# Optimization experiments

Measured on AMD Instinct MI355X. Metric: run time of the kernel, lower is better.

Reference implementation:

```python
import jax, jax.numpy as jnp
import numpy as np

N = 4000      # number_of_sensors
D_IN = 128    # input feature dim
D_OUT = 128   # output feature dim
E_DIM = 16    # node embedding dim
B = 8         # batch size


def setup_inputs() -> dict:
    key = jax.random.key(0)
    k_x, k_e1, k_e2, k_w = jax.random.split(key, 4)
    x = jax.random.normal(k_x, (B, N, D_IN), dtype=jnp.float32)
    E1 = jax.random.normal(k_e1, (N, E_DIM), dtype=jnp.float32)
    E2 = jax.random.normal(k_e2, (N, E_DIM), dtype=jnp.float32)
    W = jax.random.normal(k_w, (D_IN, D_OUT), dtype=jnp.float32) * (1.0 / np.sqrt(D_IN))
    b = jnp.zeros((D_OUT,), dtype=jnp.float32)
    return {"x": x, "E1": E1, "E2": E2, "W": W, "b": b}


def reference(x, E1, E2, W, b):
    # Adaptive adjacency from node embeddings: A = softmax(relu(E1 @ E2^T), axis=-1)
    logits = jax.nn.relu(jnp.einsum('nd,md->nm', E1, E2))  # [N, N]
    adj = jax.nn.softmax(logits, axis=-1)                  # row-normalized adjacency
    # Graph aggregation then feature transform: relu(A @ X @ W + b)
    agg = jnp.einsum('nm,bmf->bnf', adj, x)                # [B, N, D_IN]
    out = jax.nn.relu(jnp.einsum('bnf,fo->bno', agg, W) + b)  # [B, N, D_OUT]
    return out
```

## Files before the change

kernel.cpp:

```cpp
#include <hip/hip_runtime.h>
#include <hip/hip_bf16.h>

#define NSEN 4000
#define NP   4096
#define DIN  128
#define DOUT 128
#define EDIM 16
#define BATCH 8

typedef __attribute__((ext_vector_type(8))) short bf16x8;
typedef __attribute__((ext_vector_type(4))) float f32x4;

__device__ __forceinline__ unsigned short f2bf(float f) {
  unsigned int u = __float_as_uint(f);
  unsigned int r = (u + 0x7FFFu + ((u >> 16) & 1u)) >> 16;
  return (unsigned short)r;
}
__device__ __forceinline__ float bf2f(unsigned short s) {
  unsigned int u = ((unsigned int)s) << 16;
  return __uint_as_float(u);
}

__device__ __forceinline__ void gl_lds16(const void* g, void* l) {
  __builtin_amdgcn_global_load_lds((const __attribute__((address_space(1))) void*)g,
                                   (__attribute__((address_space(3))) void*)l, 16, 0, 0);
}

__global__ __launch_bounds__(512) void k_prep(const float* __restrict__ E1,
                                              const float* __restrict__ E2,
                                              const float* __restrict__ W,
                                              const float* __restrict__ x,
                                              unsigned short* __restrict__ adjp,
                                              float* __restrict__ rinv,
                                              unsigned short* __restrict__ yt) {
  __shared__ float rsum[8][16];
  __shared__ __align__(16) unsigned short pool[34816];
  const int bx = blockIdx.x;
  const int tid = threadIdx.x;
  const int lane = tid & 63, wv = tid >> 6;
  const int lr = lane & 15, lq = lane >> 4;

  if (bx >= 250) {
    unsigned short* wlds = pool;
    unsigned short* ylds = pool + 17408;
    {
      const int fr = tid >> 5;
      const int o4 = tid & 31;
#pragma unroll
      for (int r8 = 0; r8 < 8; r8++) {
        const int f = fr + r8 * 16;
        float4 w4 = *(const float4*)&W[(size_t)f * DOUT + o4 * 4];
        wlds[(o4 * 4 + 0) * 136 + f] = f2bf(w4.x);
        wlds[(o4 * 4 + 1) * 136 + f] = f2bf(w4.y);
        wlds[(o4 * 4 + 2) * 136 + f] = f2bf(w4.z);
        wlds[(o4 * 4 + 3) * 136 + f] = f2bf(w4.w);
      }
    }
    __syncthreads();

    const int yi = bx - 250;
    const int b  = yi >> 5;
    const int m0 = (yi & 31) * 128;
    const int mh = wv >> 2;
    const int os = wv & 3;

    bf16x8 af[2][4];
#pragma unroll
    for (int ot = 0; ot < 2; ot++) {
      const int ob = os * 32 + ot * 16 + lr;
#pragma unroll
      for (int ks = 0; ks < 4; ks++)
        af[ot][ks] = *(const bf16x8*)&wlds[ob * 136 + ks * 32 + lq * 8];
    }

#pragma unroll
    for (int mt = 0; mt < 4; mt++) {
      const int mloc = mh * 64 + mt * 16;
      const int m = m0 + mloc + lr;
      bf16x8 bx8[4];
      if (m < NSEN) {
        const float* xp = &x[((size_t)b * NSEN + m) * DIN + lq * 8];
#pragma unroll
        for (int ks = 0; ks < 4; ks++) {
          float4 v0 = *(const float4*)(xp + ks * 32);
          float4 v1 = *(const float4*)(xp + ks * 32 + 4);
          bx8[ks][0] = (short)f2bf(v0.x); bx8[ks][1] = (short)f2bf(v0.y);
          bx8[ks][2] = (short)f2bf(v0.z); bx8[ks][3] = (short)f2bf(v0.w);
          bx8[ks][4] = (short)f2bf(v1.x); bx8[ks][5] = (short)f2bf(v1.y);
          bx8[ks][6] = (short)f2bf(v1.z); bx8[ks][7] = (short)f2bf(v1.w);
        }
      } else {
#pragma unroll
        for (int ks = 0; ks < 4; ks++)
#pragma unroll
          for (int j = 0; j < 8; j++) bx8[ks][j] = 0;
      }
#pragma unroll
      for (int ot = 0; ot < 2; ot++) {
        f32x4 c = (f32x4){0.f, 0.f, 0.f, 0.f};
#pragma unroll
        for (int ks = 0; ks < 4; ks++)
          c = __builtin_amdgcn_mfma_f32_16x16x32_bf16(af[ot][ks], bx8[ks], c, 0, 0, 0);
#pragma unroll
        for (int i = 0; i < 4; i++)
          ylds[(os * 32 + ot * 16 + lq * 4 + i) * 136 + mloc + lr] = f2bf(c[i]);
      }
    }
    __syncthreads();
#pragma unroll
    for (int s2 = 0; s2 < 4; s2++) {
      int c = s2 * 512 + tid;
      int row = c >> 4;
      int mc = c & 15;
      *(bf16x8*)&yt[(size_t)(b * 128 + row) * NP + m0 + mc * 8] =
          *(const bf16x8*)&ylds[row * 136 + mc * 8];
    }
    return;
  }

  const int n0 = bx * 16;

  float a[8];
  {
    const float* e1p = &E1[(size_t)(n0 + lr) * EDIM + (lq & 1) * 8];
    *(float4*)&a[0] = *(const float4*)e1p;
    *(float4*)&a[4] = *(const float4*)(e1p + 4);
  }
  bf16x8 af1, af2;
#pragma unroll
  for (int j = 0; j < 8; j++) {
    unsigned short hs = f2bf(a[j]);
    af1[j] = (short)hs;
    float lo = a[j] - bf2f(hs);
    af2[j] = (lq < 2) ? (short)f2bf(lo) : (short)0;
  }

  float rs[4] = {0.f, 0.f, 0.f, 0.f};
  for (int t = wv; t < NSEN / 16; t += 8) {
    const int m = t * 16 + lr;
    float bv[8];
    const float* e2p = &E2[(size_t)m * EDIM + (lq & 1) * 8];
    *(float4*)&bv[0] = *(const float4*)e2p;
    *(float4*)&bv[4] = *(const float4*)(e2p + 4);
    bf16x8 bfrag;
#pragma unroll
    for (int j = 0; j < 8; j++) {
      unsigned short hs = f2bf(bv[j]);
      if (lq < 2) bfrag[j] = (short)hs;
      else        bfrag[j] = (short)f2bf(bv[j] - bf2f(hs));
    }
    f32x4 c = (f32x4){0.f, 0.f, 0.f, 0.f};
    c = __builtin_amdgcn_mfma_f32_16x16x32_bf16(af1, bfrag, c, 0, 0, 0);
    c = __builtin_amdgcn_mfma_f32_16x16x32_bf16(af2, bfrag, c, 0, 0, 0);
#pragma unroll
    for (int i = 0; i < 4; i++) {
      float p = __expf(fmaxf(c[i], 0.f));
      rs[i] += p;
      adjp[(size_t)(n0 + lq * 4 + i) * NP + t * 16 + lr] = f2bf(p);
    }
  }
  for (int i = tid; i < 16 * (NP - NSEN); i += 512) {
    int r = i / (NP - NSEN), c = i % (NP - NSEN);
    adjp[(size_t)(n0 + r) * NP + NSEN + c] = 0;
  }
#pragma unroll
  for (int i = 0; i < 4; i++) {
    rs[i] += __shfl_xor(rs[i], 1, 64);
    rs[i] += __shfl_xor(rs[i], 2, 64);
    rs[i] += __shfl_xor(rs[i], 4, 64);
    rs[i] += __shfl_xor(rs[i], 8, 64);
  }
  if (lr == 0) {
#pragma unroll
    for (int i = 0; i < 4; i++) rsum[wv][lq * 4 + i] = rs[i];
  }
  __syncthreads();
  if (tid < 16) {
    float s = 0.f;
#pragma unroll
    for (int w = 0; w < 8; w++) s += rsum[w][tid];
    rinv[n0 + tid] = 1.0f / s;
  }
}

__global__ __launch_bounds__(512, 2) void k_gemm(const unsigned short* __restrict__ A,
                                                 const unsigned short* __restrict__ Bt,
                                                 unsigned short* __restrict__ part,
                                                 int nsteps) {
  __shared__ __align__(16) unsigned short smem[65536];
  unsigned short* tA0 = smem;
  unsigned short* tB0 = smem + 32768;
  const int tid = threadIdx.x;
  const int lane = tid & 63, wv = tid >> 6;
  const int wr = wv >> 2, wcn = wv & 3;
  const int lr = lane & 15, lq = lane >> 4;
  const int kh = blockIdx.x >> 4;
  const int m0 = (blockIdx.x & 15) * 256;
  const int n0c = blockIdx.y * 256;
  const int kb0 = kh * nsteps * 64;

  f32x4 acc[8][4];
#pragma unroll
  for (int p = 0; p < 8; p++)
#pragma unroll
    for (int q = 0; q < 4; q++) acc[p][q] = (f32x4){0.f, 0.f, 0.f, 0.f};

#define STAGE2(bufi, kb, s)                                                             \
  {                                                                                     \
    int idx = (s) * 512 + tid;                                                          \
    int row = idx >> 3;                                                                 \
    int kc = ((idx & 7) ^ (row & 7)) << 3;                                              \
    gl_lds16(&A[(size_t)(m0 + row) * NP + (kb) + kc], &tA0[(bufi)*16384 + idx*8]);      \
    gl_lds16(&Bt[(size_t)(n0c + row) * NP + (kb) + kc], &tB0[(bufi)*16384 + idx*8]);    \
  }

  STAGE2(0, kb0, 0); STAGE2(0, kb0, 1); STAGE2(0, kb0, 2); STAGE2(0, kb0, 3);

  for (int it = 0; it < nsteps; ++it) {
    const int cur = it & 1;
    const int nxt = cur ^ 1;
    const int kbn = kb0 + (it + 1) * 64;
    const bool pf = (it < nsteps - 1);
    bf16x8 bf[4];

#pragma unroll
    for (int ks = 0; ks < 2; ks++) {
      if (ks == 0) {
        if (pf) STAGE2(nxt, kbn, 0);
        if (it == 0) { asm volatile("s_waitcnt vmcnt(0)" ::: "memory"); }
        else if (pf) { asm volatile("s_waitcnt vmcnt(2)" ::: "memory"); }
        else         { asm volatile("s_waitcnt vmcnt(0)" ::: "memory"); }
        __builtin_amdgcn_s_barrier();
      } else {
        if (pf) STAGE2(nxt, kbn, 2);
      }
      {
        const int koff = (ks * 32 + lq * 8) ^ ((lr & 7) << 3);
        bf16x8 af[4];
#pragma unroll
        for (int p = 0; p < 4; p++)
          af[p] = *(const bf16x8*)&tA0[cur * 16384 + (wr * 128 + p * 16 + lr) * 64 + koff];
#pragma unroll
        for (int q = 0; q < 4; q++)
          bf[q] = *(const bf16x8*)&tB0[cur * 16384 + (wcn * 64 + q * 16 + lr) * 64 + koff];
        if (ks == 1) __builtin_amdgcn_s_barrier();
        asm volatile("s_waitcnt lgkmcnt(0)" ::: "memory");
        __builtin_amdgcn_sched_barrier(0);
        __builtin_amdgcn_s_setprio(1);
#pragma unroll
        for (int p = 0; p < 4; p++)
#pragma unroll
          for (int q = 0; q < 4; q++)
            acc[p][q] = __builtin_amdgcn_mfma_f32_16x16x32_bf16(af[p], bf[q], acc[p][q], 0, 0, 0);
        __builtin_amdgcn_s_setprio(0);
        __builtin_amdgcn_s_barrier();
      }
      {
        if (pf) STAGE2(nxt, kbn, (ks == 0) ? 1 : 3);
        const int koff = (ks * 32 + lq * 8) ^ ((lr & 7) << 3);
        bf16x8 af[4];
#pragma unroll
        for (int p = 0; p < 4; p++)
          af[p] = *(const bf16x8*)&tA0[cur * 16384 + (wr * 128 + (4 + p) * 16 + lr) * 64 + koff];
        __builtin_amdgcn_s_barrier();
        asm volatile("s_waitcnt lgkmcnt(0)" ::: "memory");
        __builtin_amdgcn_sched_barrier(0);
        __builtin_amdgcn_s_setprio(1);
#pragma unroll
        for (int p = 0; p < 4; p++)
#pragma unroll
          for (int q = 0; q < 4; q++)
            acc[4 + p][q] = __builtin_amdgcn_mfma_f32_16x16x32_bf16(af[p], bf[q], acc[4 + p][q], 0, 0, 0);
        __builtin_amdgcn_s_setprio(0);
        __builtin_amdgcn_s_barrier();
      }
    }
  }
#undef STAGE2

  unsigned short* pdst = part + ((size_t)kh << 22);
#pragma unroll
  for (int p = 0; p < 8; p++)
#pragma unroll
    for (int q = 0; q < 4; q++) {
      const int col = n0c + wcn * 64 + q * 16 + lr;
#pragma unroll
      for (int i = 0; i < 4; i++) {
        const int row = m0 + wr * 128 + p * 16 + lq * 4 + i;
        pdst[(size_t)row * 1024 + col] = f2bf(acc[p][q][i]);
      }
    }
}

__global__ __launch_bounds__(256) void k_fin(const unsigned short* __restrict__ part,
                                             const float* __restrict__ rinv,
                                             const float* __restrict__ bias,
                                             float* __restrict__ out, int ksl) {
  const int tid = threadIdx.x;
  const int nl = tid >> 4;
  const int ch = tid & 15;
  const int n  = blockIdx.x * 16 + nl;
  const int b  = blockIdx.y;
  const int j  = b * 128 + ch * 8;

  float s[8] = {0.f, 0.f, 0.f, 0.f, 0.f, 0.f, 0.f, 0.f};
  for (int kh = 0; kh < ksl; kh++) {
    bf16x8 pv = *(const bf16x8*)&part[((size_t)kh << 22) + (size_t)n * 1024 + j];
#pragma unroll
    for (int jj = 0; jj < 8; jj++) s[jj] += bf2f((unsigned short)pv[jj]);
  }
  const float rv = rinv[n];
  float4 bb0 = *(const float4*)&bias[ch * 8];
  float4 bb1 = *(const float4*)&bias[ch * 8 + 4];
  float r[8];
#pragma unroll
  for (int jj = 0; jj < 8; jj++) {
    float bbj = (jj < 4) ? ((const float*)&bb0)[jj] : ((const float*)&bb1)[jj - 4];
    r[jj] = fmaxf(s[jj] * rv + bbj, 0.f);
  }
  float* op = &out[((size_t)b * NSEN + n) * DOUT + ch * 8];
  *(float4*)op       = make_float4(r[0], r[1], r[2], r[3]);
  *(float4*)(op + 4) = make_float4(r[4], r[5], r[6], r[7]);
}

extern "C" void kernel_launch(void* const* d_in, const int* in_sizes, int n_in,
                              void* d_out, int out_size, void* d_ws, size_t ws_size,
                              hipStream_t stream) {
  const float* x    = (const float*)d_in[0];
  const float* E1   = (const float*)d_in[1];
  const float* E2   = (const float*)d_in[2];
  const float* W    = (const float*)d_in[3];
  const float* bias = (const float*)d_in[4];
  float* out = (float*)d_out;

  char* ws = (char*)d_ws;
  unsigned short* adjp = (unsigned short*)(ws);
  unsigned short* yt   = (unsigned short*)(ws + 33554432);
  float*          rinv = (float*)(ws + 33554432 + 8388608);
  unsigned short* part = (unsigned short*)(ws + 33554432 + 8388608 + 16384);

  const size_t need4 = 33554432ull + 8388608 + 16384 + 4ull * 8388608;
  const int KS = (ws_size >= need4) ? 4 : 2;
  const int nsteps = 64 / KS;

  k_prep<<<dim3(506), dim3(512), 0, stream>>>(E1, E2, W, x, adjp, rinv, yt);
  k_gemm<<<dim3(KS * 16, 4), dim3(512), 0, stream>>>(adjp, yt, part, nsteps);
  k_fin<<<dim3(250, BATCH), dim3(256), 0, stream>>>(part, rinv, bias, out, KS);
}
```

Measured before the change: 79.28 us.

## Switch GEMM mainloop to triple-buffered K=32 stages with one barrier per step

Replaces the double-buffered K=64 LDS pipeline in the adjacency GEMM with a three-slot ring of K=32 tiles. Loads run two steps ahead, with a new XOR swizzle for 32-wide rows. Each iteration now has a single barrier instead of several. The split-K factor is also forced to 4 without checking the workspace size, which risks overrunning the buffer if the workspace is small.

```diff
diff --git a/kernel.cpp b/kernel.cpp
--- a/kernel.cpp
+++ b/kernel.cpp
@@ -187,9 +187,9 @@
                                                  const unsigned short* __restrict__ Bt,
                                                  unsigned short* __restrict__ part,
                                                  int nsteps) {
-  __shared__ __align__(16) unsigned short smem[65536];
+  __shared__ __align__(16) unsigned short smem[49152];
   unsigned short* tA0 = smem;
-  unsigned short* tB0 = smem + 32768;
+  unsigned short* tB0 = smem + 24576;
   const int tid = threadIdx.x;
   const int lane = tid & 63, wv = tid >> 6;
   const int wr = wv >> 2, wcn = wv & 3;
@@ -197,7 +197,7 @@
   const int kh = blockIdx.x >> 4;
   const int m0 = (blockIdx.x & 15) * 256;
   const int n0c = blockIdx.y * 256;
-  const int kb0 = kh * nsteps * 64;
+  const int kb0 = kh * nsteps * 32;
 
   f32x4 acc[8][4];
 #pragma unroll
@@ -205,78 +205,81 @@
 #pragma unroll
     for (int q = 0; q < 4; q++) acc[p][q] = (f32x4){0.f, 0.f, 0.f, 0.f};
 
-#define STAGE2(bufi, kb, s)                                                             \
+#define STAGE_A(sl, kb, s)                                                              \
   {                                                                                     \
     int idx = (s) * 512 + tid;                                                          \
-    int row = idx >> 3;                                                                 \
-    int kc = ((idx & 7) ^ (row & 7)) << 3;                                              \
-    gl_lds16(&A[(size_t)(m0 + row) * NP + (kb) + kc], &tA0[(bufi)*16384 + idx*8]);      \
-    gl_lds16(&Bt[(size_t)(n0c + row) * NP + (kb) + kc], &tB0[(bufi)*16384 + idx*8]);    \
-  }
-
-  STAGE2(0, kb0, 0); STAGE2(0, kb0, 1); STAGE2(0, kb0, 2); STAGE2(0, kb0, 3);
-
+    int row = idx >> 2;                                                                 \
+    int kc = (((idx & 3) ^ ((row ^ (row >> 2)) & 3)) << 3);                             \
+    gl_lds16(&A[(size_t)(m0 + row) * NP + (kb) + kc], &tA0[(sl) * 8192 + idx * 8]);     \
+  }
+#define STAGE_B(sl, kb, s)                                                              \
+  {                                                                                     \
+    int idx = (s) * 512 + tid;                                                          \
+    int row = idx >> 2;                                                                 \
+    int kc = (((idx & 3) ^ ((row ^ (row >> 2)) & 3)) << 3);                             \
+    gl_lds16(&Bt[(size_t)(n0c + row) * NP + (kb) + kc], &tB0[(sl) * 8192 + idx * 8]);   \
+  }
+
+  STAGE_A(0, kb0, 0) STAGE_A(0, kb0, 1) STAGE_B(0, kb0, 0) STAGE_B(0, kb0, 1)
+  STAGE_A(1, kb0 + 32, 0) STAGE_A(1, kb0 + 32, 1) STAGE_B(1, kb0 + 32, 0) STAGE_B(1, kb0 + 32, 1)
+
+  const int koff = ((lq ^ ((lr & 3) ^ ((lr >> 2) & 3))) << 3);
+
+  int cur = 0;
   for (int it = 0; it < nsteps; ++it) {
-    const int cur = it & 1;
-    const int nxt = cur ^ 1;
-    const int kbn = kb0 + (it + 1) * 64;
-    const bool pf = (it < nsteps - 1);
-    bf16x8 bf[4];
-
-#pragma unroll
-    for (int ks = 0; ks < 2; ks++) {
-      if (ks == 0) {
-        if (pf) STAGE2(nxt, kbn, 0);
-        if (it == 0) { asm volatile("s_waitcnt vmcnt(0)" ::: "memory"); }
-        else if (pf) { asm volatile("s_waitcnt vmcnt(2)" ::: "memory"); }
-        else         { asm volatile("s_waitcnt vmcnt(0)" ::: "memory"); }
-        __builtin_amdgcn_s_barrier();
-      } else {
-        if (pf) STAGE2(nxt, kbn, 2);
-      }
-      {
-        const int koff = (ks * 32 + lq * 8) ^ ((lr & 7) << 3);
-        bf16x8 af[4];
-#pragma unroll
-        for (int p = 0; p < 4; p++)
-          af[p] = *(const bf16x8*)&tA0[cur * 16384 + (wr * 128 + p * 16 + lr) * 64 + koff];
+    if (it < nsteps - 1) {
+      asm volatile("s_waitcnt vmcnt(4)" ::: "memory");
+    } else {
+      asm volatile("s_waitcnt vmcnt(0)" ::: "memory");
+    }
+    __builtin_amdgcn_s_barrier();
+
+    int s2 = cur + 2; if (s2 >= 3) s2 -= 3;
+    const int kbn = kb0 + (it + 2) * 32;
+    const bool pf = (it + 2 < nsteps);
+    const unsigned short* aslot = &tA0[cur * 8192];
+    const unsigned short* bslot = &tB0[cur * 8192];
+
+    bf16x8 bfr[4];
+    {
+      if (pf) { STAGE_A(s2, kbn, 0) STAGE_A(s2, kbn, 1) }
+      bf16x8 af[4];
+#pragma unroll
+      for (int p = 0; p < 4; p++)
+        af[p] = *(const bf16x8*)&aslot[(wr * 128 + p * 16 + lr) * 32 + koff];
+#pragma unroll
+      for (int q = 0; q < 4; q++)
+        bfr[q] = *(const bf16x8*)&bslot[(wcn * 64 + q * 16 + lr) * 32 + koff];
+      asm volatile("s_waitcnt lgkmcnt(0)" ::: "memory");
+      __builtin_amdgcn_sched_barrier(0);
+      __builtin_amdgcn_s_setprio(1);
+#pragma unroll
+      for (int p = 0; p < 4; p++)
 #pragma unroll
         for (int q = 0; q < 4; q++)
-          bf[q] = *(const bf16x8*)&tB0[cur * 16384 + (wcn * 64 + q * 16 + lr) * 64 + koff];
-        if (ks == 1) __builtin_amdgcn_s_barrier();
-        asm volatile("s_waitcnt lgkmcnt(0)" ::: "memory");
-        __builtin_amdgcn_sched_barrier(0);
-        __builtin_amdgcn_s_setprio(1);
-#pragma unroll
-        for (int p = 0; p < 4; p++)
-#pragma unroll
-          for (int q = 0; q < 4; q++)
-            acc[p][q] = __builtin_amdgcn_mfma_f32_16x16x32_bf16(af[p], bf[q], acc[p][q], 0, 0, 0);
-        __builtin_amdgcn_s_setprio(0);
-        __builtin_amdgcn_s_barrier();
-      }
-      {
-        if (pf) STAGE2(nxt, kbn, (ks == 0) ? 1 : 3);
-        const int koff = (ks * 32 + lq * 8) ^ ((lr & 7) << 3);
-        bf16x8 af[4];
-#pragma unroll
-        for (int p = 0; p < 4; p++)
-          af[p] = *(const bf16x8*)&tA0[cur * 16384 + (wr * 128 + (4 + p) * 16 + lr) * 64 + koff];
-        __builtin_amdgcn_s_barrier();
-        asm volatile("s_waitcnt lgkmcnt(0)" ::: "memory");
-        __builtin_amdgcn_sched_barrier(0);
-        __builtin_amdgcn_s_setprio(1);
-#pragma unroll
-        for (int p = 0; p < 4; p++)
-#pragma unroll
-          for (int q = 0; q < 4; q++)
-            acc[4 + p][q] = __builtin_amdgcn_mfma_f32_16x16x32_bf16(af[p], bf[q], acc[4 + p][q], 0, 0, 0);
-        __builtin_amdgcn_s_setprio(0);
-        __builtin_amdgcn_s_barrier();
-      }
-    }
-  }
-#undef STAGE2
+          acc[p][q] = __builtin_amdgcn_mfma_f32_16x16x32_bf16(af[p], bfr[q], acc[p][q], 0, 0, 0);
+      __builtin_amdgcn_s_setprio(0);
+    }
+    {
+      if (pf) { STAGE_B(s2, kbn, 0) STAGE_B(s2, kbn, 1) }
+      bf16x8 af[4];
+#pragma unroll
+      for (int p = 0; p < 4; p++)
+        af[p] = *(const bf16x8*)&aslot[(wr * 128 + (4 + p) * 16 + lr) * 32 + koff];
+      asm volatile("s_waitcnt lgkmcnt(0)" ::: "memory");
+      __builtin_amdgcn_sched_barrier(0);
+      __builtin_amdgcn_s_setprio(1);
+#pragma unroll
+      for (int p = 0; p < 4; p++)
+#pragma unroll
+        for (int q = 0; q < 4; q++)
+          acc[4 + p][q] = __builtin_amdgcn_mfma_f32_16x16x32_bf16(af[p], bfr[q], acc[4 + p][q], 0, 0, 0);
+      __builtin_amdgcn_s_setprio(0);
+    }
+    cur = cur + 1; if (cur >= 3) cur = 0;
+  }
+#undef STAGE_A
+#undef STAGE_B
 
   unsigned short* pdst = part + ((size_t)kh << 22);
 #pragma unroll
@@ -339,9 +342,7 @@
   float*          rinv = (float*)(ws + 33554432 + 8388608);
   unsigned short* part = (unsigned short*)(ws + 33554432 + 8388608 + 16384);
 
-  const size_t need4 = 33554432ull + 8388608 + 16384 + 4ull * 8388608;
-  const int KS = (ws_size >= need4) ? 4 : 2;
-  const int nsteps = 64 / KS;
+  const int KS = 4, nsteps = 128 / KS;
 
   k_prep<<<dim3(506), dim3(512), 0, stream>>>(E1, E2, W, x, adjp, rinv, yt);
   k_gemm<<<dim3(KS * 16, 4), dim3(512), 0, stream>>>(adjp, yt, part, nsteps);
```

Measured after the change: 80.80 us. Within noise of the previous version (+1.9%).
